# Performance work log

Hardware: AMD Instinct MI355X
Metric: run time of the kernel (lower is better)

The kernel has to match this reference:

```python
import jax, jax.numpy as jnp
import numpy as np
import math

B, Q, K, C, H, D = 4, 2048, 2048, 128, 8, 16  # c_q=c_k=c_v=C, c_hidden=D, no_heads=H


def setup_inputs() -> dict:
    key = jax.random.key(0)
    k1, k2, k3, k4, k5 = jax.random.split(key, 5)
    return {
        "q_x": jax.random.normal(k1, (B, Q, C), dtype=jnp.float32),
        "kv_x": jax.random.normal(k2, (B, K, C), dtype=jnp.float32),
        # torch Linear weight layout [out_features, in_features] = [H*D, C]
        "w_q": jax.random.normal(k3, (H * D, C), dtype=jnp.float32) * (1.0 / math.sqrt(C)),
        "w_k": jax.random.normal(k4, (H * D, C), dtype=jnp.float32) * (1.0 / math.sqrt(C)),
        "w_v": jax.random.normal(k5, (H * D, C), dtype=jnp.float32) * (1.0 / math.sqrt(C)),
    }


def reference(q_x, kv_x, w_q, w_k, w_v):
    # project + split heads: [B, S, C] x [H, D, C] -> [B, H, S, D]
    wq = w_q.reshape(H, D, C)
    wk = w_k.reshape(H, D, C)
    wv = w_v.reshape(H, D, C)
    q = jnp.einsum("bqc,hdc->bhqd", q_x, wq) / math.sqrt(D)
    k = jnp.einsum("bkc,hdc->bhkd", kv_x, wk)
    v = jnp.einsum("bkc,hdc->bhkd", kv_x, wv)
    scores = jnp.einsum("bhqd,bhkd->bhqk", q, k)  # [B, H, Q, K]
    a = jax.nn.softmax(scores, axis=-1)
    o = jnp.einsum("bhqk,bhkd->bqhd", a, v)  # transpose(-2,-3) -> [B, Q, H, D]
    return o
```

## Files before the change

### kernel.cpp

```cpp
#include <hip/hip_runtime.h>

constexpr int NB   = 4;
constexpr int SEQ  = 2048;
constexpr int CDIM = 128;
constexpr int NH   = 8;
constexpr int HD   = 16;

typedef _Float16 h_t;
typedef __attribute__((ext_vector_type(4))) _Float16 h4;
typedef __attribute__((ext_vector_type(8))) _Float16 h8;
typedef __attribute__((ext_vector_type(2))) __fp16   fp2;
typedef __attribute__((ext_vector_type(4))) float    f4;

constexpr float LOG2E = 1.44269504f;
constexpr float BIAS  = -8.0f * LOG2E;

__global__ __launch_bounds__(256)
void proj(const float* __restrict__ qx, const float* __restrict__ kvx,
          const float* __restrict__ wq, const float* __restrict__ wk,
          const float* __restrict__ wv,
          h_t* __restrict__ qh, h_t* __restrict__ kh, h_t* __restrict__ vF)
{
    const int mat = blockIdx.y;
    const int mb  = blockIdx.x * 64;
    const int wv_ = threadIdx.x >> 6;
    const int ln  = threadIdx.x & 63;
    const int r   = ln & 15, kg = ln >> 4;
    const int stile = mb + wv_ * 16;
    const int srow  = stile + r;

    const float* x = (mat == 0) ? qx : kvx;
    const float* w = (mat == 0) ? wq : (mat == 1) ? wk : wv;
    h_t*         o = (mat == 0) ? qh : (mat == 1) ? kh : vF;
    const float ws_ = (mat == 0) ? 0.25f * LOG2E : 1.0f;

    h8 xf[4];
    #pragma unroll
    for (int kc = 0; kc < 4; ++kc) {
        const float* xp = x + (size_t)srow * CDIM + kc * 32 + kg * 8;
        f4 x0 = *(const f4*)xp;
        f4 x1 = *(const f4*)(xp + 4);
        h8 tf;
        #pragma unroll
        for (int i = 0; i < 4; ++i) { tf[i] = (h_t)x0[i]; tf[4 + i] = (h_t)x1[i]; }
        xf[kc] = tf;
    }

    const int b_ = srow >> 11;
    const int s  = srow & (SEQ - 1);

    #pragma unroll
    for (int nt = 0; nt < 8; ++nt) {
        f4 acc = {0.f, 0.f, 0.f, 0.f};
        #pragma unroll
        for (int kc = 0; kc < 4; ++kc) {
            const float* wp = w + (size_t)(nt * 16 + r) * CDIM + kc * 32 + kg * 8;
            f4 w0 = *(const f4*)wp;
            f4 w1 = *(const f4*)(wp + 4);
            h8 wf;
            #pragma unroll
            for (int i = 0; i < 4; ++i) {
                wf[i]     = (h_t)(w0[i] * ws_);
                wf[4 + i] = (h_t)(w1[i] * ws_);
            }
            acc = (mat == 2)
                ? __builtin_amdgcn_mfma_f32_16x16x32_f16(xf[kc], wf, acc, 0, 0, 0)
                : __builtin_amdgcn_mfma_f32_16x16x32_f16(wf, xf[kc], acc, 0, 0, 0);
        }
        h4 pk;
        #pragma unroll
        for (int i = 0; i < 4; ++i) pk[i] = (h_t)acc[i];

        if (mat == 2) {
            const int bv = stile >> 11, sv = stile & (SEQ - 1);
            *(h4*)(o + (((size_t)bv * NH + nt) * 128 + (sv >> 4)) * 256 + r * 16 + 4 * kg) = pk;
        } else {
            *(h4*)(o + (((size_t)b_ * NH + nt) * SEQ + s) * HD + 4 * kg) = pk;
        }
    }
}

__global__ __launch_bounds__(512, 4)
void attn(const h_t* __restrict__ qh, const h_t* __restrict__ kh,
          const h_t* __restrict__ vF, float* __restrict__ out)
{
    const int bh  = blockIdx.y;
    const int w   = threadIdx.x >> 6;
    const int ws  = w & 3;
    const int kvh = w >> 2;
    const int ln  = threadIdx.x & 63;
    const int r   = ln & 15, kg = ln >> 4;

    __shared__ float oS[4][2][16][17];
    __shared__ float lS[4][2][16];

    const size_t hb = (size_t)bh * SEQ * HD;
    const int qb = blockIdx.x * 128 + ws * 32;

    h4 qf0 = *(const h4*)(qh + hb + (size_t)(qb + r)      * HD + kg * 4);
    h4 qf1 = *(const h4*)(qh + hb + (size_t)(qb + 16 + r) * HD + kg * 4);

    const h_t* kp = kh + hb + kvh * 64 * 256 + r * HD + kg * 4;
    const h_t* vp = vF + hb + kvh * 64 * 256 + r * 16 + kg * 4;

    f4 o0  = {0.f, 0.f, 0.f, 0.f}, o1  = {0.f, 0.f, 0.f, 0.f};
    f4 ol0 = {0.f, 0.f, 0.f, 0.f}, ol1 = {0.f, 0.f, 0.f, 0.f};
    const f4 cbias = {BIAS, BIAS, BIAS, BIAS};
    const h4 ones  = {(h_t)1.f, (h_t)1.f, (h_t)1.f, (h_t)1.f};

    h4 kfa = *(const h4*)(kp);
    h4 vfa = *(const h4*)(vp);
    h4 kfb = *(const h4*)(kp + 256);
    h4 vfb = *(const h4*)(vp + 256);

    for (int c = 0; c < 64; c += 2) {
        h4 kfn0 = *(const h4*)(kp + (c + 2) * 256);
        h4 vfn0 = *(const h4*)(vp + (c + 2) * 256);
        h4 kfn1 = *(const h4*)(kp + (c + 3) * 256);
        h4 vfn1 = *(const h4*)(vp + (c + 3) * 256);

        {
            f4 s0 = __builtin_amdgcn_mfma_f32_16x16x16f16(kfa, qf0, cbias, 0, 0, 0);
            f4 s1 = __builtin_amdgcn_mfma_f32_16x16x16f16(kfa, qf1, cbias, 0, 0, 0);
            const float e00 = __builtin_amdgcn_exp2f(s0[0]);
            const float e01 = __builtin_amdgcn_exp2f(s0[1]);
            const float e02 = __builtin_amdgcn_exp2f(s0[2]);
            const float e03 = __builtin_amdgcn_exp2f(s0[3]);
            const float e10 = __builtin_amdgcn_exp2f(s1[0]);
            const float e11 = __builtin_amdgcn_exp2f(s1[1]);
            const float e12 = __builtin_amdgcn_exp2f(s1[2]);
            const float e13 = __builtin_amdgcn_exp2f(s1[3]);
            union { fp2 cc[2]; h4 v; } p0, p1;
            p0.cc[0] = __builtin_amdgcn_cvt_pkrtz(e00, e01);
            p0.cc[1] = __builtin_amdgcn_cvt_pkrtz(e02, e03);
            p1.cc[0] = __builtin_amdgcn_cvt_pkrtz(e10, e11);
            p1.cc[1] = __builtin_amdgcn_cvt_pkrtz(e12, e13);
            o0  = __builtin_amdgcn_mfma_f32_16x16x16f16(p0.v, vfa,  o0,  0, 0, 0);
            ol0 = __builtin_amdgcn_mfma_f32_16x16x16f16(p0.v, ones, ol0, 0, 0, 0);
            o1  = __builtin_amdgcn_mfma_f32_16x16x16f16(p1.v, vfa,  o1,  0, 0, 0);
            ol1 = __builtin_amdgcn_mfma_f32_16x16x16f16(p1.v, ones, ol1, 0, 0, 0);
        }
        {
            f4 s0 = __builtin_amdgcn_mfma_f32_16x16x16f16(kfb, qf0, cbias, 0, 0, 0);
            f4 s1 = __builtin_amdgcn_mfma_f32_16x16x16f16(kfb, qf1, cbias, 0, 0, 0);
            const float e00 = __builtin_amdgcn_exp2f(s0[0]);
            const float e01 = __builtin_amdgcn_exp2f(s0[1]);
            const float e02 = __builtin_amdgcn_exp2f(s0[2]);
            const float e03 = __builtin_amdgcn_exp2f(s0[3]);
            const float e10 = __builtin_amdgcn_exp2f(s1[0]);
            const float e11 = __builtin_amdgcn_exp2f(s1[1]);
            const float e12 = __builtin_amdgcn_exp2f(s1[2]);
            const float e13 = __builtin_amdgcn_exp2f(s1[3]);
            union { fp2 cc[2]; h4 v; } p0, p1;
            p0.cc[0] = __builtin_amdgcn_cvt_pkrtz(e00, e01);
            p0.cc[1] = __builtin_amdgcn_cvt_pkrtz(e02, e03);
            p1.cc[0] = __builtin_amdgcn_cvt_pkrtz(e10, e11);
            p1.cc[1] = __builtin_amdgcn_cvt_pkrtz(e12, e13);
            o0  = __builtin_amdgcn_mfma_f32_16x16x16f16(p0.v, vfb,  o0,  0, 0, 0);
            ol0 = __builtin_amdgcn_mfma_f32_16x16x16f16(p0.v, ones, ol0, 0, 0, 0);
            o1  = __builtin_amdgcn_mfma_f32_16x16x16f16(p1.v, vfb,  o1,  0, 0, 0);
            ol1 = __builtin_amdgcn_mfma_f32_16x16x16f16(p1.v, ones, ol1, 0, 0, 0);
        }

        kfa = kfn0; vfa = vfn0;
        kfb = kfn1; vfb = vfn1;
    }

    if (kvh == 1) {
        #pragma unroll
        for (int reg = 0; reg < 4; ++reg) {
            oS[ws][0][4 * kg + reg][r] = o0[reg];
            oS[ws][1][4 * kg + reg][r] = o1[reg];
        }
        if (r == 0) {
            #pragma unroll
            for (int reg = 0; reg < 4; ++reg) {
                lS[ws][0][4 * kg + reg] = ol0[reg];
                lS[ws][1][4 * kg + reg] = ol1[reg];
            }
        }
    }
    __syncthreads();

    if (kvh == 0) {
        const int b_ = bh >> 3, h = bh & 7;
        #pragma unroll
        for (int reg = 0; reg < 4; ++reg) {
            const int row = 4 * kg + reg;
            const float O0 = o0[reg] + oS[ws][0][row][r];
            const float O1 = o1[reg] + oS[ws][1][row][r];
            const float L0 = ol0[reg] + lS[ws][0][row];
            const float L1 = ol1[reg] + lS[ws][1][row];
            const int q0 = qb + row;
            const int q1 = q0 + 16;
            out[(((size_t)b_ * SEQ + q0) * NH + h) * HD + r] = O0 / L0;
            out[(((size_t)b_ * SEQ + q1) * NH + h) * HD + r] = O1 / L1;
        }
    }
}

extern "C" void kernel_launch(void* const* d_in, const int* in_sizes, int n_in,
                              void* d_out, int out_size, void* d_ws, size_t ws_size,
                              hipStream_t stream) {
    const float* qx  = (const float*)d_in[0];
    const float* kvx = (const float*)d_in[1];
    const float* wq  = (const float*)d_in[2];
    const float* wk  = (const float*)d_in[3];
    const float* wv  = (const float*)d_in[4];
    float* out = (float*)d_out;

    const size_t per = (size_t)NB * NH * SEQ * HD;
    h_t* qp = (h_t*)d_ws;
    h_t* kp = qp + per;
    h_t* vp = kp + per;

    proj<<<dim3(128, 3), dim3(256), 0, stream>>>(qx, kvx, wq, wk, wv, qp, kp, vp);
    attn<<<dim3(16, 32), dim3(512), 0, stream>>>(qp, kp, vp, out);
}
```

Baseline: 104.2 us.

## Split attention KV range four ways per block and double the grid

Each attention block now covers 64 queries split over 2 query-wave groups. The KV sequence is split four ways across waves instead of two, and partial outputs are reduced through larger shared arrays. The grid doubles to 1024 blocks, and the launch-bounds occupancy hint rises from 4 to 8. This aims at more parallelism and shorter per-wave loops, in exchange for K/V loads being shared across fewer queries (more memory traffic) and a larger shared-memory reduction.

```diff
diff --git a/kernel.cpp b/kernel.cpp
--- a/kernel.cpp
+++ b/kernel.cpp
@@ -80,28 +80,28 @@
     }
 }
 
-__global__ __launch_bounds__(512, 4)
+__global__ __launch_bounds__(512, 8)
 void attn(const h_t* __restrict__ qh, const h_t* __restrict__ kh,
           const h_t* __restrict__ vF, float* __restrict__ out)
 {
     const int bh  = blockIdx.y;
     const int w   = threadIdx.x >> 6;
-    const int ws  = w & 3;
-    const int kvh = w >> 2;
+    const int qs  = w & 1;
+    const int kvq = w >> 1;
     const int ln  = threadIdx.x & 63;
     const int r   = ln & 15, kg = ln >> 4;
 
-    __shared__ float oS[4][2][16][17];
-    __shared__ float lS[4][2][16];
+    __shared__ float oS[2][3][2][16][17];
+    __shared__ float lS[2][3][2][16];
 
     const size_t hb = (size_t)bh * SEQ * HD;
-    const int qb = blockIdx.x * 128 + ws * 32;
+    const int qb = blockIdx.x * 64 + qs * 32;
 
     h4 qf0 = *(const h4*)(qh + hb + (size_t)(qb + r)      * HD + kg * 4);
     h4 qf1 = *(const h4*)(qh + hb + (size_t)(qb + 16 + r) * HD + kg * 4);
 
-    const h_t* kp = kh + hb + kvh * 64 * 256 + r * HD + kg * 4;
-    const h_t* vp = vF + hb + kvh * 64 * 256 + r * 16 + kg * 4;
+    const h_t* kp = kh + hb + kvq * 32 * 256 + r * HD + kg * 4;
+    const h_t* vp = vF + hb + kvq * 32 * 256 + r * 16 + kg * 4;
 
     f4 o0  = {0.f, 0.f, 0.f, 0.f}, o1  = {0.f, 0.f, 0.f, 0.f};
     f4 ol0 = {0.f, 0.f, 0.f, 0.f}, ol1 = {0.f, 0.f, 0.f, 0.f};
@@ -113,7 +113,7 @@
     h4 kfb = *(const h4*)(kp + 256);
     h4 vfb = *(const h4*)(vp + 256);
 
-    for (int c = 0; c < 64; c += 2) {
+    for (int c = 0; c < 32; c += 2) {
         h4 kfn0 = *(const h4*)(kp + (c + 2) * 256);
         h4 vfn0 = *(const h4*)(vp + (c + 2) * 256);
         h4 kfn1 = *(const h4*)(kp + (c + 3) * 256);
@@ -166,31 +166,37 @@
         kfb = kfn1; vfb = vfn1;
     }
 
-    if (kvh == 1) {
+    if (kvq != 0) {
+        const int slot = kvq - 1;
         #pragma unroll
         for (int reg = 0; reg < 4; ++reg) {
-            oS[ws][0][4 * kg + reg][r] = o0[reg];
-            oS[ws][1][4 * kg + reg][r] = o1[reg];
+            oS[qs][slot][0][4 * kg + reg][r] = o0[reg];
+            oS[qs][slot][1][4 * kg + reg][r] = o1[reg];
         }
         if (r == 0) {
             #pragma unroll
             for (int reg = 0; reg < 4; ++reg) {
-                lS[ws][0][4 * kg + reg] = ol0[reg];
-                lS[ws][1][4 * kg + reg] = ol1[reg];
+                lS[qs][slot][0][4 * kg + reg] = ol0[reg];
+                lS[qs][slot][1][4 * kg + reg] = ol1[reg];
             }
         }
     }
     __syncthreads();
 
-    if (kvh == 0) {
+    if (kvq == 0) {
         const int b_ = bh >> 3, h = bh & 7;
         #pragma unroll
         for (int reg = 0; reg < 4; ++reg) {
             const int row = 4 * kg + reg;
-            const float O0 = o0[reg] + oS[ws][0][row][r];
-            const float O1 = o1[reg] + oS[ws][1][row][r];
-            const float L0 = ol0[reg] + lS[ws][0][row];
-            const float L1 = ol1[reg] + lS[ws][1][row];
+            float O0 = o0[reg], O1 = o1[reg];
+            float L0 = ol0[reg], L1 = ol1[reg];
+            #pragma unroll
+            for (int sl = 0; sl < 3; ++sl) {
+                O0 += oS[qs][sl][0][row][r];
+                O1 += oS[qs][sl][1][row][r];
+                L0 += lS[qs][sl][0][row];
+                L1 += lS[qs][sl][1][row];
+            }
             const int q0 = qb + row;
             const int q1 = q0 + 16;
             out[(((size_t)b_ * SEQ + q0) * NH + h) * HD + r] = O0 / L0;
@@ -215,5 +221,5 @@
     h_t* vp = kp + per;
 
     proj<<<dim3(128, 3), dim3(256), 0, stream>>>(qx, kvx, wq, wk, wv, qp, kp, vp);
-    attn<<<dim3(16, 32), dim3(512), 0, stream>>>(qp, kp, vp, out);
+    attn<<<dim3(32, 32), dim3(512), 0, stream>>>(qp, kp, vp, out);
 }
```

New measurement: 102.8 us. About the same (-1.4%).
